# Optimization experiments

Hardware: AMD Instinct MI355X
Metric: run time of the kernel (lower is better)

The kernel has to match this reference:

```python
import jax, jax.numpy as jnp
import numpy as np
import math

B, H, W, DM = 4, 64, 64, 96
DS, DCONV, EXPAND = 16, 3, 2
DI = EXPAND * DM
DTR = math.ceil(DM / 16)
K = 4
HID = 4 * DI


def layernorm(x, g, b, eps=1e-5):
    m = x.mean(-1, keepdims=True)
    v = ((x - m) ** 2).mean(-1, keepdims=True)
    return (x - m) / jnp.sqrt(v + eps) * g + b


def dwconv(x, w, b=None):
    # x: (B,C,H,W), w: (C,1,kh,kw) depthwise, odd kernel => SAME padding == k//2
    out = jax.lax.conv_general_dilated(x, w, (1, 1), 'SAME',
                                       feature_group_count=x.shape[1],
                                       dimension_numbers=('NCHW', 'OIHW', 'NCHW'))
    if b is not None:
        out = out + b[None, :, None, None]
    return out


def ss2d_core(xc, x_proj_w, dt_projs_w, dt_projs_b, A_logs, Ds):
    # xc: (b, d_inner, h, w) -> (b, d_inner, L) summed over 4 scan directions
    b, c, h, w = xc.shape
    L = h * w
    x_hw = xc.reshape(b, c, L)
    x_wh = xc.transpose(0, 1, 3, 2).reshape(b, c, L)
    xs = jnp.stack([x_hw, x_wh], axis=1)                 # (b,2,c,L)
    xs = jnp.concatenate([xs, jnp.flip(xs, -1)], axis=1)  # (b,4,c,L)
    x_dbl = jnp.einsum('bkdl,kcd->bkcl', xs, x_proj_w)
    dts, Bs, Cs = jnp.split(x_dbl, [DTR, DTR + DS], axis=2)
    dts = jnp.einsum('bkrl,kdr->bkdl', dts, dt_projs_w)
    delta = jax.nn.softplus(dts + dt_projs_b[None, :, :, None])  # (b,K,c,L)
    A = -jnp.exp(A_logs).reshape(K, c, DS)                       # (K,c,n)

    def step(hst, inp):
        x_t, d_t, B_t, C_t = inp  # (b,K,c),(b,K,c),(b,K,n),(b,K,n)
        dA = jnp.exp(d_t[..., None] * A)                       # (b,K,c,n)
        hst = hst * dA + (d_t * x_t)[..., None] * B_t[:, :, None, :]
        y = jnp.einsum('bkdn,bkn->bkd', hst, C_t)
        return hst, y

    seq = (jnp.moveaxis(xs, -1, 0), jnp.moveaxis(delta, -1, 0),
           jnp.moveaxis(Bs, -1, 0), jnp.moveaxis(Cs, -1, 0))
    h0 = jnp.zeros((b, K, c, DS), xc.dtype)
    _, ys = jax.lax.scan(step, h0, seq)          # (L,b,K,c)
    ys = jnp.moveaxis(ys, 0, -1)                 # (b,K,c,L)
    ys = ys + Ds.reshape(K, c)[None, :, :, None] * xs
    y1 = ys[:, 0]
    inv = jnp.flip(ys[:, 2:4], -1)
    y2 = inv[:, 0]
    wh = ys[:, 1].reshape(b, c, w, h).swapaxes(2, 3).reshape(b, c, L)
    invwh = inv[:, 1].reshape(b, c, w, h).swapaxes(2, 3).reshape(b, c, L)
    return y1 + y2 + wh + invwh


def msffn(y, in_w, in_b, dw1, dw3, dw5, ln_g, ln_b, out_w, out_b):
    hcl = jax.nn.silu(y @ in_w.T + in_b)          # (b,h,w,HID)
    hc = hcl.transpose(0, 3, 1, 2)
    hc = hc + dwconv(hc, dw1) + dwconv(hc, dw3) + dwconv(hc, dw5)
    hn = layernorm(hc.transpose(0, 2, 3, 1), ln_g, ln_b)
    return hn @ out_w.T + out_b


def setup_inputs() -> dict:
    key = jax.random.key(0)
    ks = jax.random.split(key, 16)
    dt_init_std = DTR ** -0.5
    dt = jnp.exp(jax.random.uniform(ks[0], (K, DI)) * (math.log(0.1) - math.log(0.001)) + math.log(0.001))
    dt = jnp.clip(dt, 1e-4, None)
    inv_dt = dt + jnp.log(-jnp.expm1(-dt))          # softplus-inverse init for dt bias
    A_logs = jnp.tile(jnp.log(jnp.arange(1, DS + 1, dtype=jnp.float32))[None, :], (K * DI, 1))
    r = lambda i, sh, s: jax.random.normal(ks[i], sh, jnp.float32) * s
    return {
        'x': r(1, (B, H, W, DM), 1.0),
        'in_proj_w': r(2, (2 * DI, DM), DM ** -0.5),
        'conv_w': r(3, (DI, 1, DCONV, DCONV), 0.2),
        'conv_b': jnp.zeros((DI,), jnp.float32),
        'x_proj_w': r(4, (K, DTR + 2 * DS, DI), DI ** -0.5),
        'dt_projs_w': jax.random.uniform(ks[5], (K, DI, DTR), minval=-dt_init_std, maxval=dt_init_std),
        'dt_projs_b': inv_dt,
        'A_logs': A_logs,
        'Ds': jnp.ones((K * DI,), jnp.float32),
        'out_norm_g': jnp.ones((DI,), jnp.float32),
        'out_norm_b': jnp.zeros((DI,), jnp.float32),
        'out_proj_w': r(6, (DM, DI), DI ** -0.5),
        'ffn_in_w': r(7, (HID, DI), DI ** -0.5),
        'ffn_in_b': jnp.zeros((HID,), jnp.float32),
        'ffn_dw1': r(8, (HID, 1, 1, 1), 0.3),
        'ffn_dw3': r(9, (HID, 1, 3, 3), 0.2),
        'ffn_dw5': r(10, (HID, 1, 5, 5), 0.1),
        'ffn_ln_g': jnp.ones((HID,), jnp.float32),
        'ffn_ln_b': jnp.zeros((HID,), jnp.float32),
        'ffn_out_w': r(11, (DM, HID), HID ** -0.5),
        'ffn_out_b': jnp.zeros((DM,), jnp.float32),
        'skip_scale': jnp.ones((1,), jnp.float32),
    }


def reference(x, in_proj_w, conv_w, conv_b, x_proj_w, dt_projs_w, dt_projs_b, A_logs, Ds,
              out_norm_g, out_norm_b, out_proj_w, ffn_in_w, ffn_in_b, ffn_dw1, ffn_dw3,
              ffn_dw5, ffn_ln_g, ffn_ln_b, ffn_out_w, ffn_out_b, skip_scale):
    b, h, w, _ = x.shape
    xz = x @ in_proj_w.T                          # (b,h,w,2*DI)
    xi, z = jnp.split(xz, 2, axis=-1)
    xc = jax.nn.silu(dwconv(xi.transpose(0, 3, 1, 2), conv_w, conv_b))  # (b,DI,h,w)
    y = ss2d_core(xc, x_proj_w, dt_projs_w, dt_projs_b, A_logs, Ds)     # (b,DI,L)
    y = y.swapaxes(1, 2).reshape(b, h, w, DI)
    y = layernorm(y, out_norm_g, out_norm_b)
    y = y * jax.nn.silu(z)
    out = y @ out_proj_w.T
    ffn = msffn(y, ffn_in_w, ffn_in_b, ffn_dw1, ffn_dw3, ffn_dw5,
                ffn_ln_g, ffn_ln_b, ffn_out_w, ffn_out_b)
    return out + skip_scale * ffn
```

## Files before the change

kernel.cpp:

```cpp
#include <hip/hip_runtime.h>
#include <hip/hip_bf16.h>

constexpr int BB = 4, HH = 64, WW = 64, DMv = 96;
constexpr int DSn = 16, DIv = 192, DTRv = 6, KKv = 4, HIDv = 768;
constexpr int LL = 4096;
constexpr int NC = 32, CHK = LL / NC;
constexpr int NR = BB * LL;
constexpr int XDS = 40;

constexpr size_t S_xi   = (size_t)BB * LL * DIv;
constexpr size_t S_xdbl = (size_t)BB * KKv * LL * XDS;
constexpr size_t S_big  = (size_t)BB * KKv * LL * DIv;
constexpr size_t S_sp   = (size_t)BB * KKv * NC * DIv * DSn;

typedef __attribute__((ext_vector_type(8))) short short8;
typedef __attribute__((ext_vector_type(4))) float floatx4;

__device__ __forceinline__ float sigf(float x) { return 1.f / (1.f + __expf(-x)); }
__device__ __forceinline__ float softp(float x) {
  return (x > 20.f) ? x : __logf(1.f + __expf(x));
}
__device__ __forceinline__ short bfbits(float v) {
  __hip_bfloat16 h = __float2bfloat16(v);
  return *(short*)&h;
}

__device__ __forceinline__ int lmap(int k, int l) {
  int lr = (k & 2) ? (LL - 1 - l) : l;
  return (k & 1) ? (((lr & 63) << 6) | (lr >> 6)) : lr;
}

__global__ void k_wprep(const float* __restrict__ fiw, const float* __restrict__ opw,
                        const float* __restrict__ fow, const float* __restrict__ in_w,
                        const float* __restrict__ xpw, const float* __restrict__ x,
                        float* __restrict__ fiwT, float* __restrict__ opwT,
                        float* __restrict__ fowT, float* __restrict__ wt,
                        float* __restrict__ wcatT, float* __restrict__ xt,
                        short* __restrict__ fiwP) {
  int bx = blockIdx.x, t = threadIdx.x;
  __shared__ float smbuf[32 * 65];
  if (bx >= 1152) {
    int f = (bx - 1152) * 4 + (t >> 6);
    int lane = t & 63, ln16 = lane & 15, qd = lane >> 4;
    int kt = f / 48, ntg = f % 48;
    int n = ntg * 16 + ln16;
#pragma unroll
    for (int j = 0; j < 8; ++j) {
      int k = kt * 32 + qd * 8 + j;
      fiwP[(size_t)f * 512 + lane * 8 + j] = bfbits(fiw[(size_t)n * DIv + k]);
    }
    return;
  }
  if (bx >= 384) {
    int i4 = bx - 384;
    int r0 = (i4 / 3) * 64, k0 = (i4 % 3) * 32;
    float (*tile)[65] = (float(*)[65])smbuf;
#pragma unroll
    for (int ii = 0; ii < 8; ++ii) {
      int i = (t >> 5) + ii * 8, j = t & 31;
      tile[j][i] = x[(size_t)(r0 + i) * 96 + k0 + j];
    }
    __syncthreads();
#pragma unroll
    for (int jj = 0; jj < 8; ++jj) {
      int j = (t >> 6) + jj * 4, i = t & 63;
      xt[(size_t)(k0 + j) * NR + r0 + i] = tile[j][i];
    }
    return;
  }
  if (bx >= 270) {
    int idx = (bx - 270) * 256 + t;
    if (idx < 2 * 192 * 76) {
      int p = idx / (192 * 76);
      int rem = idx % (192 * 76);
      int d = rem / 76, j = rem % 76;
      int k = (j >= 38 ? 2 : 0) + p;
      int c = (j >= 38) ? j - 38 : j;
      wcatT[idx] = xpw[((size_t)(k * 38 + c)) * DIv + d];
    }
    return;
  }
  const float* src; float* dst; int R, C, r0, c0;
  if (bx < 144)      { src = fiw;  dst = fiwT; R = 768; C = 192; r0 = (bx / 6) * 32;         c0 = (bx % 6) * 32; }
  else if (bx < 162) { int i = bx - 144; src = opw; dst = opwT; R = 96;  C = 192; r0 = (i / 6) * 32;  c0 = (i % 6) * 32; }
  else if (bx < 234) { int i = bx - 162; src = fow; dst = fowT; R = 96;  C = 768; r0 = (i / 24) * 32; c0 = (i % 24) * 32; }
  else               { int i = bx - 234; src = in_w; dst = wt;  R = 384; C = 96;  r0 = (i / 3) * 32;  c0 = (i % 3) * 32; }
  float (*tile)[33] = (float(*)[33])smbuf;
  int tc = t & 31, tr = t >> 5;
#pragma unroll
  for (int i = 0; i < 4; ++i) {
    int r = r0 + tr + i * 8;
    if (r < R && c0 + tc < C) tile[tr + i * 8][tc] = src[(size_t)r * C + c0 + tc];
  }
  __syncthreads();
#pragma unroll
  for (int i = 0; i < 4; ++i) {
    int c = c0 + tr + i * 8;
    int r = r0 + tc;
    if (c < C && r < R) dst[(size_t)c * R + r] = tile[tc][tr + i * 8];
  }
}

__global__ void k_inproj(const float* __restrict__ xt, const float* __restrict__ wt,
                         float* __restrict__ xi, float* __restrict__ z) {
  int t = threadIdx.x;
  int wv = t >> 6, lane = t & 63;
  int rq = blockIdx.x * 256 + wv * 64 + lane;
  int c0 = blockIdx.y * 8;
  const float4* xt4 = (const float4*)xt;
  float4 acc[8];
#pragma unroll
  for (int c = 0; c < 8; ++c) acc[c] = make_float4(0.f, 0.f, 0.f, 0.f);
  for (int k = 0; k < 96; ++k) {
    float4 xv = xt4[(size_t)k * (NR / 4) + rq];
    const float* wr = wt + k * 384 + c0;
#pragma unroll
    for (int c = 0; c < 8; ++c) {
      float w = wr[c];
      acc[c].x += w * xv.x; acc[c].y += w * xv.y;
      acc[c].z += w * xv.z; acc[c].w += w * xv.w;
    }
  }
  float* dst; int cc;
  if (c0 < DIv) { dst = xi; cc = c0; } else { dst = z; cc = c0 - DIv; }
#pragma unroll
  for (int li = 0; li < 4; ++li) {
    size_t row = (size_t)rq * 4 + li;
    float4 v0, v1;
    v0.x = (&acc[0].x)[li]; v0.y = (&acc[1].x)[li];
    v0.z = (&acc[2].x)[li]; v0.w = (&acc[3].x)[li];
    v1.x = (&acc[4].x)[li]; v1.y = (&acc[5].x)[li];
    v1.z = (&acc[6].x)[li]; v1.w = (&acc[7].x)[li];
    float4* o4 = (float4*)(dst + row * DIv + cc);
    o4[0] = v0; o4[1] = v1;
  }
}

constexpr int TW2 = 18;
__global__ void k_dwconv3(const float* __restrict__ xi, const float* __restrict__ cw,
                          const float* __restrict__ cb, float* __restrict__ xc,
                          float* __restrict__ xcT, float* __restrict__ xcTs) {
  int tile = blockIdx.x;
  int cg = blockIdx.y, b = blockIdx.z;
  int t = threadIdx.x;
  int ti0 = (tile >> 2) * 16, tj0 = (tile & 3) * 16;
  __shared__ float sm[TW2 * TW2 * 32];

  for (int e = t; e < TW2 * TW2 * 32; e += 256) {
    int ec = e & 31;
    int sp = e >> 5;
    int hi = sp / TW2, hj = sp % TW2;
    int gi = ti0 + hi - 1, gj = tj0 + hj - 1;
    float v = 0.f;
    if ((unsigned)gi < (unsigned)HH && (unsigned)gj < (unsigned)WW)
      v = xi[((size_t)b * LL + gi * WW + gj) * DIv + cg * 32 + ec];
    sm[e] = v;
  }

  int c = t & 31, s0 = t >> 5;
  int cglob = cg * 32 + c;
  float wc[9];
#pragma unroll
  for (int j = 0; j < 9; ++j) wc[j] = cw[cglob * 9 + j];
  float bv = cb[cglob];
  __syncthreads();

  float res[32];
  for (int i = 0; i < 32; ++i) {
    int p = s0 + (i << 3);
    int r = p >> 4, q = p & 15;
    float s = bv;
#pragma unroll
    for (int di = 0; di < 3; ++di)
#pragma unroll
      for (int dj = 0; dj < 3; ++dj)
        s += sm[((r + di) * TW2 + (q + dj)) * 32 + c] * wc[di * 3 + dj];
    res[i] = s * sigf(s);
  }
  __syncthreads();
  for (int i = 0; i < 32; ++i) {
    int p = s0 + (i << 3);
    sm[p * 35 + c] = res[i];
  }
  __syncthreads();
  for (int it = 0; it < 32; ++it) {
    int e = it * 256 + t;
    int p = e >> 5, ec = e & 31;
    int l = (ti0 + (p >> 4)) * WW + tj0 + (p & 15);
    xc[((size_t)b * LL + l) * DIv + cg * 32 + ec] = sm[p * 35 + ec];
  }
  for (int d2 = 0; d2 < 32; ++d2) {
    int l = (ti0 + (t >> 4)) * WW + tj0 + (t & 15);
    xcT[(size_t)(cg * 32 + d2) * NR + b * LL + l] = sm[t * 35 + d2];
  }
  for (int d2 = 0; d2 < 32; ++d2) {
    int gjo = t >> 4, gio = t & 15;
    int lt2 = (tj0 + gjo) * WW + ti0 + gio;
    int p = gio * 16 + gjo;
    xcTs[(size_t)(cg * 32 + d2) * NR + b * LL + lt2] = sm[p * 35 + d2];
  }
}

__global__ void k_xdbl2(const float* __restrict__ xcT, const float* __restrict__ xcTs,
                        const float* __restrict__ wcatT, float* __restrict__ xdbl) {
  int t = threadIdx.x;
  int rq = blockIdx.x * 256 + t;
  int jg = blockIdx.y;
  int pb = blockIdx.z;
  int p = pb >> 2, b = pb & 3;
  const float4* A = (const float4*)(p ? xcTs : xcT);
  const float* wbase = wcatT + (size_t)p * 192 * 76 + jg * 4;
  float4 acc[4];
#pragma unroll
  for (int j = 0; j < 4; ++j) acc[j] = make_float4(0.f, 0.f, 0.f, 0.f);
  for (int d = 0; d < 192; ++d) {
    float4 xv = A[(size_t)d * (NR / 4) + b * 1024 + rq];
    const float* wr = wbase + d * 76;
#pragma unroll
    for (int j = 0; j < 4; ++j) {
      float w = wr[j];
      acc[j].x += w * xv.x; acc[j].y += w * xv.y;
      acc[j].z += w * xv.z; acc[j].w += w * xv.w;
    }
  }
#pragma unroll
  for (int li = 0; li < 4; ++li) {
    int r = rq * 4 + li;
#pragma unroll
    for (int j = 0; j < 4; ++j) {
      int col = jg * 4 + j;
      int kk = (col >= 38) ? (2 + p) : p;
      int c = (col >= 38) ? col - 38 : col;
      int l = (col >= 38) ? (LL - 1 - r) : r;
      int phys = c + (c >= 6 ? 2 : 0);
      size_t ro = (((size_t)(b * KKv + kk)) * LL + l) * XDS;
      xdbl[ro + phys] = (&acc[j].x)[li];
      if (col == 5) { xdbl[ro + 6] = 0.f; xdbl[ro + 7] = 0.f; }
    }
  }
}

__global__ void k_scan1(const float* __restrict__ xdbl, const float* __restrict__ xc,
                        const float* __restrict__ alogs, const float* __restrict__ dtw,
                        const float* __restrict__ dtb,
                        float* __restrict__ S, float* __restrict__ P) {
  int bx = blockIdx.x;
  int c = bx / 3, dblk = bx % 3;
  int k = blockIdx.y, b = blockIdx.z;
  int t = threadIdx.x, dl = t >> 2, nq = t & 3;
  int d = dblk * 64 + dl;
  __shared__ float de_s[16][64], xv_s[16][64], bc_s[16][32], dt_s[16][8];
  float A[4];
#pragma unroll
  for (int j = 0; j < 4; ++j)
    A[j] = -__expf(alogs[(size_t)(k * DIv + d) * DSn + nq * 4 + j]);
  int derow = t >> 4, dec0 = (t & 15) * 4;
  float DTW[4][6], DTB[4];
#pragma unroll
  for (int jj = 0; jj < 4; ++jj) {
    int dd = k * DIv + dblk * 64 + dec0 + jj;
    DTB[jj] = dtb[dd];
#pragma unroll
    for (int r2 = 0; r2 < 6; ++r2) DTW[jj][r2] = dtw[(size_t)dd * 6 + r2];
  }
  size_t bkL = (size_t)(b * KKv + k) * LL;
  const float* xq = xdbl + bkL * XDS;
  const float* xcb = xc + (size_t)b * LL * DIv;
  float h[4] = {0.f, 0.f, 0.f, 0.f}, sA[4] = {0.f, 0.f, 0.f, 0.f};
  int l0 = c * CHK;
  for (int tile = 0; tile < CHK / 16; ++tile) {
    int lt = l0 + tile * 16;
    __syncthreads();
    {
      int r = t >> 4, q = t & 15;
      int lc = lmap(k, lt + r);
      *(float4*)&xv_s[r][q * 4] = *(const float4*)(xcb + (size_t)lc * DIv + dblk * 64 + q * 4);
      if (t < 128) {
        int r2 = t >> 3, q2 = t & 7;
        *(float4*)&bc_s[r2][q2 * 4] = *(const float4*)(xq + (size_t)(lt + r2) * XDS + 8 + q2 * 4);
      } else if (t < 160) {
        int i3 = t - 128, r3 = i3 >> 1, half = i3 & 1;
        *(float4*)&dt_s[r3][half * 4] = *(const float4*)(xq + (size_t)(lt + r3) * XDS + half * 4);
      }
    }
    __syncthreads();
    {
#pragma unroll
      for (int jj = 0; jj < 4; ++jj) {
        float s = DTB[jj];
#pragma unroll
        for (int r2 = 0; r2 < 6; ++r2) s += dt_s[derow][r2] * DTW[jj][r2];
        de_s[derow][dec0 + jj] = softp(s);
      }
    }
    __syncthreads();
#pragma unroll
    for (int i2 = 0; i2 < 16; ++i2) {
      float de = de_s[i2][dl];
      float xv = xv_s[i2][dl];
      float4 Bv = *(float4*)&bc_s[i2][nq * 4];
      float db = de * xv;
#pragma unroll
      for (int j = 0; j < 4; ++j) {
        float u = de * A[j];
        sA[j] += u;
        h[j] = h[j] * __expf(u) + db * (&Bv.x)[j];
      }
    }
  }
  size_t o = ((((size_t)(b * KKv + k) * NC + c) * 3 + dblk) * 1024) + (size_t)t * 4;
  float4 hs, ps;
#pragma unroll
  for (int j = 0; j < 4; ++j) { (&hs.x)[j] = h[j]; (&ps.x)[j] = __expf(sA[j]); }
  *(float4*)(S + o) = hs;
  *(float4*)(P + o) = ps;
}

__global__ void k_scan2(float* __restrict__ S, const float* __restrict__ P) {
  int dblk = blockIdx.x, k = blockIdx.y, b = blockIdx.z;
  int t = threadIdx.x;
  size_t base = (((size_t)(b * KKv + k) * NC) * 3 + dblk) * 1024 + (size_t)t * 4;
  float4 h = make_float4(0.f, 0.f, 0.f, 0.f);
  for (int c = 0; c < NC; ++c) {
    size_t o = base + (size_t)c * 3 * 1024;
    float4 s = *(float4*)(S + o), p = *(float4*)(P + o);
    *(float4*)(S + o) = h;
    h.x = s.x + p.x * h.x; h.y = s.y + p.y * h.y;
    h.z = s.z + p.z * h.z; h.w = s.w + p.w * h.w;
  }
}

__global__ void k_scan3(const float* __restrict__ xdbl, const float* __restrict__ xc,
                        const float* __restrict__ alogs, const float* __restrict__ dtw,
                        const float* __restrict__ dtb,
                        const float* __restrict__ Hin, float* __restrict__ ys) {
  int bx = blockIdx.x;
  int c = bx / 3, dblk = bx % 3;
  int k = blockIdx.y, b = blockIdx.z;
  int t = threadIdx.x, dl = t >> 2, nq = t & 3;
  int d = dblk * 64 + dl;
  __shared__ float de_s[16][64], xv_s[16][64], bc_s[16][32], dt_s[16][8];
  float A[4];
#pragma unroll
  for (int j = 0; j < 4; ++j)
    A[j] = -__expf(alogs[(size_t)(k * DIv + d) * DSn + nq * 4 + j]);
  int derow = t >> 4, dec0 = (t & 15) * 4;
  float DTW[4][6], DTB[4];
#pragma unroll
  for (int jj = 0; jj < 4; ++jj) {
    int dd = k * DIv + dblk * 64 + dec0 + jj;
    DTB[jj] = dtb[dd];
#pragma unroll
    for (int r2 = 0; r2 < 6; ++r2) DTW[jj][r2] = dtw[(size_t)dd * 6 + r2];
  }
  size_t bkL = (size_t)(b * KKv + k) * LL;
  const float* xq = xdbl + bkL * XDS;
  const float* xcb = xc + (size_t)b * LL * DIv;
  float* yp = ys + bkL * DIv + d;
  size_t o = ((((size_t)(b * KKv + k) * NC + c) * 3 + dblk) * 1024) + (size_t)t * 4;
  float4 h4 = *(const float4*)(Hin + o);
  float h[4] = {h4.x, h4.y, h4.z, h4.w};
  int l0 = c * CHK;
  for (int tile = 0; tile < CHK / 16; ++tile) {
    int lt = l0 + tile * 16;
    __syncthreads();
    {
      int r = t >> 4, q = t & 15;
      int lc = lmap(k, lt + r);
      *(float4*)&xv_s[r][q * 4] = *(const float4*)(xcb + (size_t)lc * DIv + dblk * 64 + q * 4);
      if (t < 128) {
        int r2 = t >> 3, q2 = t & 7;
        *(float4*)&bc_s[r2][q2 * 4] = *(const float4*)(xq + (size_t)(lt + r2) * XDS + 8 + q2 * 4);
      } else if (t < 160) {
        int i3 = t - 128, r3 = i3 >> 1, half = i3 & 1;
        *(float4*)&dt_s[r3][half * 4] = *(const float4*)(xq + (size_t)(lt + r3) * XDS + half * 4);
      }
    }
    __syncthreads();
    {
#pragma unroll
      for (int jj = 0; jj < 4; ++jj) {
        float s = DTB[jj];
#pragma unroll
        for (int r2 = 0; r2 < 6; ++r2) s += dt_s[derow][r2] * DTW[jj][r2];
        de_s[derow][dec0 + jj] = softp(s);
      }
    }
    __syncthreads();
#pragma unroll
    for (int i2 = 0; i2 < 16; ++i2) {
      float de = de_s[i2][dl];
      float xv = xv_s[i2][dl];
      float4 Bv = *(float4*)&bc_s[i2][nq * 4];
      float4 Cv = *(float4*)&bc_s[i2][16 + nq * 4];
      float db = de * xv;
      float p = 0.f;
#pragma unroll
      for (int j = 0; j < 4; ++j) {
        h[j] = h[j] * __expf(de * A[j]) + db * (&Bv.x)[j];
        p += h[j] * (&Cv.x)[j];
      }
      p += __shfl_down(p, 2, 4);
      p += __shfl_down(p, 1, 4);
      if (nq == 0) yp[(size_t)(lt + i2) * DIv] = p;
    }
  }
}

__global__ void k_comlnt(const float* __restrict__ ys, const float* __restrict__ xc,
                         const float* __restrict__ Ds, const float* __restrict__ z,
                         const float* __restrict__ g, const float* __restrict__ be,
                         float* __restrict__ ygtT, __hip_bfloat16* __restrict__ ygtB) {
  int bl0 = blockIdx.x * 32;
  int b = bl0 >> 12, l0 = bl0 & 4095;
  int t = threadIdx.x;
  __shared__ float vbuf[32 * 193];
  __shared__ float m_[32], rs_[32];
  __shared__ float tile[32][33];
  {
    int grp = t >> 6, lane6 = t & 63;
    size_t base = (size_t)b * KKv * LL * DIv;
#pragma unroll
    for (int i8 = 0; i8 < 8; ++i8) {
      int li = grp + i8 * 4;
      int l = l0 + li;
      int lT = ((l & 63) << 6) | (l >> 6);
      const float* r0 = ys + base + (size_t)l * DIv;
      const float* r2 = ys + base + ((size_t)2 * LL + (LL - 1 - l)) * DIv;
      const float* r1 = ys + base + ((size_t)1 * LL + lT) * DIv;
      const float* r3 = ys + base + ((size_t)3 * LL + (LL - 1 - lT)) * DIv;
      const float* xr = xc + ((size_t)b * LL + l) * DIv;
#pragma unroll
      for (int cc = 0; cc < 3; ++cc) {
        int d = lane6 + cc * 64;
        float sd = Ds[d] + Ds[DIv + d] + Ds[2 * DIv + d] + Ds[3 * DIv + d];
        vbuf[li * 193 + d] = r0[d] + r2[d] + r1[d] + r3[d] + sd * xr[d];
      }
    }
  }
  __syncthreads();
  {
    int r = t >> 3, q = t & 7;
    float s = 0.f, qq = 0.f;
#pragma unroll
    for (int j = 0; j < 24; ++j) {
      float v = vbuf[r * 193 + q + j * 8];
      s += v; qq += v * v;
    }
    s += __shfl_down(s, 4, 8); qq += __shfl_down(qq, 4, 8);
    s += __shfl_down(s, 2, 8); qq += __shfl_down(qq, 2, 8);
    s += __shfl_down(s, 1, 8); qq += __shfl_down(qq, 1, 8);
    if (q == 0) {
      float m = s / DIv;
      m_[r] = m;
      rs_[r] = rsqrtf(qq / DIv - m * m + 1e-5f);
    }
  }
  __syncthreads();
  int tc = t & 31, tr = t >> 5;
  for (int ch = 0; ch < 6; ++ch) {
    int c0 = ch * 32;
    float gg = g[c0 + tc], bb = be[c0 + tc];
    if (ch) __syncthreads();
#pragma unroll
    for (int i = 0; i < 4; ++i) {
      int r = tr + i * 8;
      float v = vbuf[r * 193 + c0 + tc];
      float zz = z[(size_t)(bl0 + r) * DIv + c0 + tc];
      float val = (v - m_[r]) * rs_[r] * gg + bb;
      float gated = val * zz * sigf(zz);
      tile[tc][r] = gated;
      ygtB[(size_t)(bl0 + r) * DIv + c0 + tc] = __float2bfloat16(gated);
    }
    __syncthreads();
#pragma unroll
    for (int i = 0; i < 4; ++i) {
      int cr = tr + i * 8;
      ygtT[(size_t)(c0 + cr) * NR + bl0 + tc] = tile[cr][tc];
    }
  }
}

__global__ void k_outp(const float* __restrict__ ygtT, const float* __restrict__ opwT,
                       float* __restrict__ out0) {
  int t = threadIdx.x;
  int r2 = blockIdx.x * 256 + t;
  int c0 = blockIdx.y * 4;
  const float2* x2 = (const float2*)ygtT;
  float2 acc[4];
#pragma unroll
  for (int c = 0; c < 4; ++c) acc[c] = make_float2(0.f, 0.f);
#pragma unroll 4
  for (int k = 0; k < DIv; ++k) {
    float2 xv = x2[(size_t)k * (NR / 2) + r2];
    const float* wr = opwT + k * DMv + c0;
#pragma unroll
    for (int c = 0; c < 4; ++c) {
      float w = wr[c];
      acc[c].x += w * xv.x; acc[c].y += w * xv.y;
    }
  }
#pragma unroll
  for (int li = 0; li < 2; ++li) {
    float4 v;
    v.x = (&acc[0].x)[li]; v.y = (&acc[1].x)[li];
    v.z = (&acc[2].x)[li]; v.w = (&acc[3].x)[li];
    *(float4*)(out0 + ((size_t)r2 * 2 + li) * DMv + c0) = v;
  }
}

__global__ void k_ffnmf(const __hip_bfloat16* __restrict__ ygtB,
                        const short* __restrict__ fiwP,
                        const float* __restrict__ bias, float* __restrict__ hcl) {
  int t = threadIdx.x;
  int wv = t >> 6, lane = t & 63;
  int ln16 = lane & 15, qd = lane >> 4;
  int m0 = blockIdx.x * 64 + wv * 16;
  int n0 = blockIdx.y * 64;
  int ntg0 = n0 >> 4;
  floatx4 acc[4];
  floatx4 zero4 = {0.f, 0.f, 0.f, 0.f};
#pragma unroll
  for (int nt = 0; nt < 4; ++nt) acc[nt] = zero4;
  const short* arow = (const short*)ygtB + (size_t)(m0 + ln16) * DIv + qd * 8;
#pragma unroll
  for (int kt = 0; kt < 6; ++kt) {
    short8 a = *(const short8*)(arow + kt * 32);
    const short* bb = fiwP + ((size_t)(kt * 48 + ntg0) * 64 + lane) * 8;
#pragma unroll
    for (int nt = 0; nt < 4; ++nt) {
      short8 bfr = *(const short8*)(bb + (size_t)nt * 512);
      acc[nt] = __builtin_amdgcn_mfma_f32_16x16x32_bf16(a, bfr, acc[nt], 0, 0, 0);
    }
  }
#pragma unroll
  for (int nt = 0; nt < 4; ++nt) {
    int col = n0 + nt * 16 + ln16;
    float bv = bias[col];
#pragma unroll
    for (int r = 0; r < 4; ++r) {
      int row = m0 + qd * 4 + r;
      float s = acc[nt][r] + bv;
      hcl[(size_t)row * HIDv + col] = s * sigf(s);
    }
  }
}

constexpr int TS = 16, CG = 32, TW = TS + 4;
__global__ void k_ffnconv2(const float* __restrict__ hcl, const float* __restrict__ w1,
                           const float* __restrict__ w3, const float* __restrict__ w5,
                           float* __restrict__ hc2) {
  int tile = blockIdx.x;
  int cg = blockIdx.y, b = blockIdx.z;
  int t = threadIdx.x;
  int ti0 = (tile >> 2) * TS, tj0 = (tile & 3) * TS;
  __shared__ float sm[TW * TW * CG];

  for (int e = t; e < TW * TW * CG; e += 256) {
    int ec = e & 31;
    int sp = e >> 5;
    int hi = sp / TW, hj = sp % TW;
    int gi = ti0 + hi - 2, gj = tj0 + hj - 2;
    float v = 0.f;
    if ((unsigned)gi < (unsigned)HH && (unsigned)gj < (unsigned)WW)
      v = hcl[((size_t)b * LL + gi * WW + gj) * HIDv + cg * CG + ec];
    sm[e] = v;
  }

  int c = t & 31;
  int cglob = cg * CG + c;
  float wc[25];
#pragma unroll
  for (int di = 0; di < 5; ++di)
#pragma unroll
    for (int dj = 0; dj < 5; ++dj) {
      float w = w5[cglob * 25 + di * 5 + dj];
      if (di >= 1 && di <= 3 && dj >= 1 && dj <= 3)
        w += w3[cglob * 9 + (di - 1) * 3 + (dj - 1)];
      if (di == 2 && dj == 2) w += 1.f + w1[cglob];
      wc[di * 5 + dj] = w;
    }
  __syncthreads();

  int q2 = t >> 5;
#pragma unroll
  for (int half = 0; half < 2; ++half) {
    int q = q2 + half * 8;
    float win[5][5];
#pragma unroll
    for (int di = 0; di < 4; ++di)
#pragma unroll
      for (int dj = 0; dj < 5; ++dj)
        win[di][dj] = sm[(di * TW + (q + dj)) * CG + c];
#pragma unroll
    for (int r = 0; r < 16; ++r) {
      int slot = (r + 4) % 5;
#pragma unroll
      for (int dj = 0; dj < 5; ++dj)
        win[slot][dj] = sm[(((r + 4) * TW) + (q + dj)) * CG + c];
      float s = 0.f;
#pragma unroll
      for (int di = 0; di < 5; ++di) {
        int wsl = (r + di) % 5;
#pragma unroll
        for (int dj = 0; dj < 5; ++dj)
          s += win[wsl][dj] * wc[di * 5 + dj];
      }
      hc2[((size_t)b * LL + (ti0 + r) * WW + (tj0 + q)) * HIDv + cglob] = s;
    }
  }
}

__global__ void k_ln2t(const float* __restrict__ hc2, const float* __restrict__ g,
                       const float* __restrict__ be, float* __restrict__ hnT) {
  int r0 = blockIdx.x * 32;
  int t = threadIdx.x;
  __shared__ float m_[32], rs_[32];
  __shared__ float tile[32][33];
  {
    int r = t >> 3, q = t & 7;
    const float4* row4 = (const float4*)(hc2 + (size_t)(r0 + r) * HIDv);
    float s = 0.f, qq = 0.f;
#pragma unroll
    for (int j = 0; j < 24; ++j) {
      float4 v = row4[q + j * 8];
      s += v.x + v.y + v.z + v.w;
      qq += v.x * v.x + v.y * v.y + v.z * v.z + v.w * v.w;
    }
    s += __shfl_down(s, 4, 8); qq += __shfl_down(qq, 4, 8);
    s += __shfl_down(s, 2, 8); qq += __shfl_down(qq, 2, 8);
    s += __shfl_down(s, 1, 8); qq += __shfl_down(qq, 1, 8);
    if (q == 0) {
      float m = s / HIDv;
      m_[r] = m;
      rs_[r] = rsqrtf(qq / HIDv - m * m + 1e-5f);
    }
  }
  __syncthreads();
  int tc = t & 31, tr = t >> 5;
  for (int ch = 0; ch < 24; ++ch) {
    int c0 = ch * 32;
    float gg = g[c0 + tc], bb = be[c0 + tc];
    if (ch) __syncthreads();
#pragma unroll
    for (int i = 0; i < 4; ++i) {
      int r = tr + i * 8;
      float v = hc2[(size_t)(r0 + r) * HIDv + c0 + tc];
      tile[tc][r] = (v - m_[r]) * rs_[r] * gg + bb;
    }
    __syncthreads();
#pragma unroll
    for (int i = 0; i < 4; ++i) {
      int cr = tr + i * 8;
      hnT[(size_t)(c0 + cr) * NR + r0 + tc] = tile[cr][tc];
    }
  }
}

__global__ void k_final3(const float* __restrict__ hnT, const float* __restrict__ fowT,
                         float* __restrict__ part) {
  int t = threadIdx.x;
  int rq = blockIdx.x * 128 + t;
  int c0 = blockIdx.y * 8;
  int ks = blockIdx.z;
  const float4* x4 = (const float4*)hnT;
  float4 acc[8];
#pragma unroll
  for (int c = 0; c < 8; ++c) acc[c] = make_float4(0.f, 0.f, 0.f, 0.f);
  int k0 = ks * 192;
#pragma unroll 4
  for (int k = k0; k < k0 + 192; ++k) {
    float4 xv = x4[(size_t)k * (NR / 4) + rq];
    const float* wr = fowT + k * DMv + c0;
#pragma unroll
    for (int c = 0; c < 8; ++c) {
      float w = wr[c];
      acc[c].x += w * xv.x; acc[c].y += w * xv.y;
      acc[c].z += w * xv.z; acc[c].w += w * xv.w;
    }
  }
  float* pb = part + (size_t)ks * NR * DMv;
#pragma unroll
  for (int li = 0; li < 4; ++li) {
    size_t row = (size_t)rq * 4 + li;
#pragma unroll
    for (int cc = 0; cc < 2; ++cc) {
      float4 v;
#pragma unroll
      for (int j = 0; j < 4; ++j) (&v.x)[j] = (&acc[cc * 4 + j].x)[li];
      *(float4*)(pb + row * DMv + c0 + cc * 4) = v;
    }
  }
}

__global__ void k_finred(const float* __restrict__ part, const float* __restrict__ out0,
                         const float* __restrict__ bias, const float* __restrict__ skip,
                         float* __restrict__ dout) {
  size_t i = (size_t)blockIdx.x * 256 + threadIdx.x;
  int cq = (int)(i % (DMv / 4));
  const float4* p4 = (const float4*)part;
  size_t npart = (size_t)NR * DMv / 4;
  float4 a = p4[i], b2 = p4[i + npart], c2 = p4[i + 2 * npart], d2 = p4[i + 3 * npart];
  float4 o = ((const float4*)out0)[i];
  float4 bi = ((const float4*)bias)[cq];
  float sk = skip[0];
  float4 r;
  r.x = o.x + sk * (a.x + b2.x + c2.x + d2.x + bi.x);
  r.y = o.y + sk * (a.y + b2.y + c2.y + d2.y + bi.y);
  r.z = o.z + sk * (a.z + b2.z + c2.z + d2.z + bi.z);
  r.w = o.w + sk * (a.w + b2.w + c2.w + d2.w + bi.w);
  ((float4*)dout)[i] = r;
}

extern "C" void kernel_launch(void* const* d_in, const int* in_sizes, int n_in,
                              void* d_out, int out_size, void* d_ws, size_t ws_size,
                              hipStream_t stream) {
  const float* x        = (const float*)d_in[0];
  const float* in_w     = (const float*)d_in[1];
  const float* conv_w   = (const float*)d_in[2];
  const float* conv_b   = (const float*)d_in[3];
  const float* xpw      = (const float*)d_in[4];
  const float* dtw      = (const float*)d_in[5];
  const float* dtb      = (const float*)d_in[6];
  const float* alogs    = (const float*)d_in[7];
  const float* Ds       = (const float*)d_in[8];
  const float* ong      = (const float*)d_in[9];
  const float* onb      = (const float*)d_in[10];
  const float* opw      = (const float*)d_in[11];
  const float* fiw      = (const float*)d_in[12];
  const float* fib      = (const float*)d_in[13];
  const float* dw1      = (const float*)d_in[14];
  const float* dw3      = (const float*)d_in[15];
  const float* dw5      = (const float*)d_in[16];
  const float* flg      = (const float*)d_in[17];
  const float* flb      = (const float*)d_in[18];
  const float* fow      = (const float*)d_in[19];
  const float* fob      = (const float*)d_in[20];
  const float* skip     = (const float*)d_in[21];

  float* ws    = (float*)d_ws;
  float* xi    = ws;
  float* z     = xi + S_xi;
  float* xc    = z + S_xi;
  float* xdbl  = xc + S_xi;
  float* scr   = xdbl + S_xdbl;
  float* ys    = scr + S_big;
  float* wtiny = ys + S_big;
  float* fiwT  = wtiny;
  float* opwT  = fiwT + 147456;
  float* fowT  = opwT + 18432;
  float* wcatT = fowT + 73728;
  float* wt    = wcatT + 29184;
  __hip_bfloat16* ygtB = (__hip_bfloat16*)(wt + 36864);
  short* fiwP  = (short*)((float*)(wt + 36864) + 1572864);

  float* xt = scr;
  k_wprep<<<1224, 256, 0, stream>>>(fiw, opw, fow, in_w, xpw, x,
                                    fiwT, opwT, fowT, wt, wcatT, xt, fiwP);

  dim3 gip(NR / 1024, 48);
  k_inproj<<<gip, 256, 0, stream>>>(xt, wt, xi, z);

  float* xcT  = ys;
  float* xcTs = ys + S_xi;
  dim3 gdw(16, DIv / 32, BB);
  k_dwconv3<<<gdw, 256, 0, stream>>>(xi, conv_w, conv_b, xc, xcT, xcTs);

  dim3 gxd(4, 19, 8);
  k_xdbl2<<<gxd, 256, 0, stream>>>(xcT, xcTs, wcatT, xdbl);

  float* Sbuf = xi;
  float* Pbuf = xi + S_sp;
  dim3 gs13(NC * 3, KKv, BB);
  dim3 gs2(3, KKv, BB);
  k_scan1<<<gs13, 256, 0, stream>>>(xdbl, xc, alogs, dtw, dtb, Sbuf, Pbuf);
  k_scan2<<<gs2, 256, 0, stream>>>(Sbuf, Pbuf);
  k_scan3<<<gs13, 256, 0, stream>>>(xdbl, xc, alogs, dtw, dtb, Sbuf, ys);

  float* ygtT = xi;
  k_comlnt<<<NR / 32, 256, 0, stream>>>(ys, xc, Ds, z, ong, onb, ygtT, ygtB);

  float* out0 = xdbl;
  float* hcl = scr;
  dim3 gop(NR / 512, DMv / 4);
  k_outp<<<gop, 256, 0, stream>>>(ygtT, opwT, out0);
  dim3 gmf(NR / 64, HIDv / 64);
  k_ffnmf<<<gmf, 256, 0, stream>>>(ygtB, fiwP, fib, hcl);

  float* hc2 = ys;
  dim3 gc(16, HIDv / CG, BB);
  k_ffnconv2<<<gc, 256, 0, stream>>>(hcl, dw1, dw3, dw5, hc2);

  float* hnT = scr;
  k_ln2t<<<NR / 32, 256, 0, stream>>>(hc2, flg, flb, hnT);

  float* part = xi;
  dim3 gfn(NR / 512, DMv / 8, 4);
  k_final3<<<gfn, 128, 0, stream>>>(hnT, fowT, part);
  k_finred<<<(NR * DMv / 4) / 256, 256, 0, stream>>>(part, out0, fob, skip, (float*)d_out);
}
```

Baseline: 471.9 us.

## Fuse out-proj and FFN output GEMMs into one split-bf16 MFMA kernel

Replaces the scalar fp32 out-projection, the transposed LN2 output, the split-K final GEMM and the reduction kernel with one MFMA kernel. That kernel computes both GEMMs using bf16 hi/lo splitting (three MFMAs per tile) and writes the final output directly. LN2 and the gating kernel now write row-major bf16 hi/lo pairs instead of fp32 transposed buffers. Weight prep packs opw/fow into MFMA fragment layout and drops the unused transposes. The aim is to cut scalar FMA work, the partial-sum traffic and two launches, at the cost of slightly reduced precision from the bf16x3 emulation.

Result: faster. 430.9 us (-8.7%).

```diff
diff --git a/kernel.cpp b/kernel.cpp
--- a/kernel.cpp
+++ b/kernel.cpp
@@ -14,6 +14,7 @@
 constexpr size_t S_sp   = (size_t)BB * KKv * NC * DIv * DSn;
 
 typedef __attribute__((ext_vector_type(8))) short short8;
+typedef __attribute__((ext_vector_type(4))) short short4v;
 typedef __attribute__((ext_vector_type(4))) float floatx4;
 
 __device__ __forceinline__ float sigf(float x) { return 1.f / (1.f + __expf(-x)); }
@@ -33,43 +34,26 @@
 __global__ void k_wprep(const float* __restrict__ fiw, const float* __restrict__ opw,
                         const float* __restrict__ fow, const float* __restrict__ in_w,
                         const float* __restrict__ xpw, const float* __restrict__ x,
-                        float* __restrict__ fiwT, float* __restrict__ opwT,
-                        float* __restrict__ fowT, float* __restrict__ wt,
-                        float* __restrict__ wcatT, float* __restrict__ xt,
-                        short* __restrict__ fiwP) {
+                        float* __restrict__ wt, float* __restrict__ wcatT,
+                        float* __restrict__ xt, short* __restrict__ fiwP,
+                        short* __restrict__ opwP, short* __restrict__ fowP) {
   int bx = blockIdx.x, t = threadIdx.x;
   __shared__ float smbuf[32 * 65];
-  if (bx >= 1152) {
-    int f = (bx - 1152) * 4 + (t >> 6);
-    int lane = t & 63, ln16 = lane & 15, qd = lane >> 4;
-    int kt = f / 48, ntg = f % 48;
-    int n = ntg * 16 + ln16;
-#pragma unroll
-    for (int j = 0; j < 8; ++j) {
-      int k = kt * 32 + qd * 8 + j;
-      fiwP[(size_t)f * 512 + lane * 8 + j] = bfbits(fiw[(size_t)n * DIv + k]);
-    }
+  if (bx < 36) {
+    int r0 = (bx / 3) * 32, c0 = (bx % 3) * 32;
+    float (*tile)[33] = (float(*)[33])smbuf;
+    int tc = t & 31, tr = t >> 5;
+#pragma unroll
+    for (int i = 0; i < 4; ++i)
+      tile[tr + i * 8][tc] = in_w[(size_t)(r0 + tr + i * 8) * 96 + c0 + tc];
+    __syncthreads();
+#pragma unroll
+    for (int i = 0; i < 4; ++i)
+      wt[(size_t)(c0 + tr + i * 8) * 384 + r0 + tc] = tile[tc][tr + i * 8];
     return;
   }
-  if (bx >= 384) {
-    int i4 = bx - 384;
-    int r0 = (i4 / 3) * 64, k0 = (i4 % 3) * 32;
-    float (*tile)[65] = (float(*)[65])smbuf;
-#pragma unroll
-    for (int ii = 0; ii < 8; ++ii) {
-      int i = (t >> 5) + ii * 8, j = t & 31;
-      tile[j][i] = x[(size_t)(r0 + i) * 96 + k0 + j];
-    }
-    __syncthreads();
-#pragma unroll
-    for (int jj = 0; jj < 8; ++jj) {
-      int j = (t >> 6) + jj * 4, i = t & 63;
-      xt[(size_t)(k0 + j) * NR + r0 + i] = tile[j][i];
-    }
-    return;
-  }
-  if (bx >= 270) {
-    int idx = (bx - 270) * 256 + t;
+  if (bx < 150) {
+    int idx = (bx - 36) * 256 + t;
     if (idx < 2 * 192 * 76) {
       int p = idx / (192 * 76);
       int rem = idx % (192 * 76);
@@ -80,24 +64,63 @@
     }
     return;
   }
-  const float* src; float* dst; int R, C, r0, c0;
-  if (bx < 144)      { src = fiw;  dst = fiwT; R = 768; C = 192; r0 = (bx / 6) * 32;         c0 = (bx % 6) * 32; }
-  else if (bx < 162) { int i = bx - 144; src = opw; dst = opwT; R = 96;  C = 192; r0 = (i / 6) * 32;  c0 = (i % 6) * 32; }
-  else if (bx < 234) { int i = bx - 162; src = fow; dst = fowT; R = 96;  C = 768; r0 = (i / 24) * 32; c0 = (i % 24) * 32; }
-  else               { int i = bx - 234; src = in_w; dst = wt;  R = 384; C = 96;  r0 = (i / 3) * 32;  c0 = (i % 3) * 32; }
-  float (*tile)[33] = (float(*)[33])smbuf;
-  int tc = t & 31, tr = t >> 5;
-#pragma unroll
-  for (int i = 0; i < 4; ++i) {
-    int r = r0 + tr + i * 8;
-    if (r < R && c0 + tc < C) tile[tr + i * 8][tc] = src[(size_t)r * C + c0 + tc];
-  }
-  __syncthreads();
-#pragma unroll
-  for (int i = 0; i < 4; ++i) {
-    int c = c0 + tr + i * 8;
-    int r = r0 + tc;
-    if (c < C && r < R) dst[(size_t)c * R + r] = tile[tc][tr + i * 8];
+  if (bx < 918) {
+    int i4 = bx - 150;
+    int r0 = (i4 / 3) * 64, k0 = (i4 % 3) * 32;
+    float (*tile)[65] = (float(*)[65])smbuf;
+#pragma unroll
+    for (int ii = 0; ii < 8; ++ii) {
+      int i = (t >> 5) + ii * 8, j = t & 31;
+      tile[j][i] = x[(size_t)(r0 + i) * 96 + k0 + j];
+    }
+    __syncthreads();
+#pragma unroll
+    for (int jj = 0; jj < 8; ++jj) {
+      int j = (t >> 6) + jj * 4, i = t & 63;
+      xt[(size_t)(k0 + j) * NR + r0 + i] = tile[j][i];
+    }
+    return;
+  }
+  int lane = t & 63, ln16 = lane & 15, qd = lane >> 4;
+  if (bx < 990) {
+    int f = (bx - 918) * 4 + (t >> 6);
+    int kt = f / 48, ntg = f % 48;
+    int n = ntg * 16 + ln16;
+#pragma unroll
+    for (int j = 0; j < 8; ++j) {
+      int k = kt * 32 + qd * 8 + j;
+      fiwP[(size_t)f * 512 + lane * 8 + j] = bfbits(fiw[(size_t)n * DIv + k]);
+    }
+    return;
+  }
+  if (bx < 1008) {
+    int u = (bx - 990) * 4 + (t >> 6);
+    int f = u >> 1, part = u & 1;
+    int kt = f / 6, ntg = f % 6;
+    int n = ntg * 16 + ln16;
+#pragma unroll
+    for (int j = 0; j < 8; ++j) {
+      int k = kt * 32 + qd * 8 + j;
+      float w = opw[(size_t)n * DIv + k];
+      __hip_bfloat16 h = __float2bfloat16(w);
+      float v = part ? (w - (float)h) : w;
+      opwP[((size_t)(part * 36 + f)) * 512 + lane * 8 + j] = bfbits(v);
+    }
+    return;
+  }
+  {
+    int u = (bx - 1008) * 4 + (t >> 6);
+    int f = u >> 1, part = u & 1;
+    int kt = f / 6, ntg = f % 6;
+    int n = ntg * 16 + ln16;
+#pragma unroll
+    for (int j = 0; j < 8; ++j) {
+      int k = kt * 32 + qd * 8 + j;
+      float w = fow[(size_t)n * HIDv + k];
+      __hip_bfloat16 h = __float2bfloat16(w);
+      float v = part ? (w - (float)h) : w;
+      fowP[((size_t)(part * 144 + f)) * 512 + lane * 8 + j] = bfbits(v);
+    }
   }
 }
 
@@ -410,13 +433,13 @@
 __global__ void k_comlnt(const float* __restrict__ ys, const float* __restrict__ xc,
                          const float* __restrict__ Ds, const float* __restrict__ z,
                          const float* __restrict__ g, const float* __restrict__ be,
-                         float* __restrict__ ygtT, __hip_bfloat16* __restrict__ ygtB) {
+                         __hip_bfloat16* __restrict__ ygtB,
+                         __hip_bfloat16* __restrict__ ygtBl) {
   int bl0 = blockIdx.x * 32;
   int b = bl0 >> 12, l0 = bl0 & 4095;
   int t = threadIdx.x;
   __shared__ float vbuf[32 * 193];
   __shared__ float m_[32], rs_[32];
-  __shared__ float tile[32][33];
   {
     int grp = t >> 6, lane6 = t & 63;
     size_t base = (size_t)b * KKv * LL * DIv;
@@ -458,10 +481,10 @@
   }
   __syncthreads();
   int tc = t & 31, tr = t >> 5;
+#pragma unroll
   for (int ch = 0; ch < 6; ++ch) {
     int c0 = ch * 32;
     float gg = g[c0 + tc], bb = be[c0 + tc];
-    if (ch) __syncthreads();
 #pragma unroll
     for (int i = 0; i < 4; ++i) {
       int r = tr + i * 8;
@@ -469,43 +492,10 @@
       float zz = z[(size_t)(bl0 + r) * DIv + c0 + tc];
       float val = (v - m_[r]) * rs_[r] * gg + bb;
       float gated = val * zz * sigf(zz);
-      tile[tc][r] = gated;
-      ygtB[(size_t)(bl0 + r) * DIv + c0 + tc] = __float2bfloat16(gated);
-    }
-    __syncthreads();
-#pragma unroll
-    for (int i = 0; i < 4; ++i) {
-      int cr = tr + i * 8;
-      ygtT[(size_t)(c0 + cr) * NR + bl0 + tc] = tile[cr][tc];
-    }
-  }
-}
-
-__global__ void k_outp(const float* __restrict__ ygtT, const float* __restrict__ opwT,
-                       float* __restrict__ out0) {
-  int t = threadIdx.x;
-  int r2 = blockIdx.x * 256 + t;
-  int c0 = blockIdx.y * 4;
-  const float2* x2 = (const float2*)ygtT;
-  float2 acc[4];
-#pragma unroll
-  for (int c = 0; c < 4; ++c) acc[c] = make_float2(0.f, 0.f);
-#pragma unroll 4
-  for (int k = 0; k < DIv; ++k) {
-    float2 xv = x2[(size_t)k * (NR / 2) + r2];
-    const float* wr = opwT + k * DMv + c0;
-#pragma unroll
-    for (int c = 0; c < 4; ++c) {
-      float w = wr[c];
-      acc[c].x += w * xv.x; acc[c].y += w * xv.y;
-    }
-  }
-#pragma unroll
-  for (int li = 0; li < 2; ++li) {
-    float4 v;
-    v.x = (&acc[0].x)[li]; v.y = (&acc[1].x)[li];
-    v.z = (&acc[2].x)[li]; v.w = (&acc[3].x)[li];
-    *(float4*)(out0 + ((size_t)r2 * 2 + li) * DMv + c0) = v;
+      __hip_bfloat16 h = __float2bfloat16(gated);
+      ygtB[(size_t)(bl0 + r) * DIv + c0 + tc] = h;
+      ygtBl[(size_t)(bl0 + r) * DIv + c0 + tc] = __float2bfloat16(gated - (float)h);
+    }
   }
 }
 
@@ -611,25 +601,34 @@
   }
 }
 
-__global__ void k_ln2t(const float* __restrict__ hc2, const float* __restrict__ g,
-                       const float* __restrict__ be, float* __restrict__ hnT) {
-  int r0 = blockIdx.x * 32;
+constexpr int LNROWS = 16, LNPAD = 776;
+__global__ void k_ln2b(const float* __restrict__ hc2, const float* __restrict__ g,
+                       const float* __restrict__ be,
+                       short* __restrict__ hnBh, short* __restrict__ hnBl) {
+  int r0 = blockIdx.x * LNROWS;
   int t = threadIdx.x;
-  __shared__ float m_[32], rs_[32];
-  __shared__ float tile[32][33];
+  __shared__ float rows[LNROWS * LNPAD];
+  __shared__ float m_[LNROWS], rs_[LNROWS];
+#pragma unroll
+  for (int i = 0; i < 12; ++i) {
+    int idx4 = t + i * 256;
+    int row = idx4 / 192, c4 = idx4 % 192;
+    float4 v = *(const float4*)(hc2 + (size_t)(r0 + row) * HIDv + c4 * 4);
+    *(float4*)&rows[row * LNPAD + c4 * 4] = v;
+  }
+  __syncthreads();
   {
-    int r = t >> 3, q = t & 7;
-    const float4* row4 = (const float4*)(hc2 + (size_t)(r0 + r) * HIDv);
+    int r = t >> 4, q = t & 15;
     float s = 0.f, qq = 0.f;
 #pragma unroll
-    for (int j = 0; j < 24; ++j) {
-      float4 v = row4[q + j * 8];
-      s += v.x + v.y + v.z + v.w;
-      qq += v.x * v.x + v.y * v.y + v.z * v.z + v.w * v.w;
-    }
-    s += __shfl_down(s, 4, 8); qq += __shfl_down(qq, 4, 8);
-    s += __shfl_down(s, 2, 8); qq += __shfl_down(qq, 2, 8);
-    s += __shfl_down(s, 1, 8); qq += __shfl_down(qq, 1, 8);
+    for (int j = 0; j < 48; ++j) {
+      float v = rows[r * LNPAD + q + j * 16];
+      s += v; qq += v * v;
+    }
+    s += __shfl_down(s, 8, 16); qq += __shfl_down(qq, 8, 16);
+    s += __shfl_down(s, 4, 16); qq += __shfl_down(qq, 4, 16);
+    s += __shfl_down(s, 2, 16); qq += __shfl_down(qq, 2, 16);
+    s += __shfl_down(s, 1, 16); qq += __shfl_down(qq, 1, 16);
     if (q == 0) {
       float m = s / HIDv;
       m_[r] = m;
@@ -637,79 +636,88 @@
     }
   }
   __syncthreads();
-  int tc = t & 31, tr = t >> 5;
-  for (int ch = 0; ch < 24; ++ch) {
-    int c0 = ch * 32;
-    float gg = g[c0 + tc], bb = be[c0 + tc];
-    if (ch) __syncthreads();
-#pragma unroll
-    for (int i = 0; i < 4; ++i) {
-      int r = tr + i * 8;
-      float v = hc2[(size_t)(r0 + r) * HIDv + c0 + tc];
-      tile[tc][r] = (v - m_[r]) * rs_[r] * gg + bb;
-    }
-    __syncthreads();
-#pragma unroll
-    for (int i = 0; i < 4; ++i) {
-      int cr = tr + i * 8;
-      hnT[(size_t)(c0 + cr) * NR + r0 + tc] = tile[cr][tc];
-    }
-  }
-}
-
-__global__ void k_final3(const float* __restrict__ hnT, const float* __restrict__ fowT,
-                         float* __restrict__ part) {
+#pragma unroll
+  for (int i = 0; i < 12; ++i) {
+    int idx4 = t + i * 256;
+    int row = idx4 / 192, c4 = idx4 % 192;
+    float4 v = *(const float4*)&rows[row * LNPAD + c4 * 4];
+    float4 gv = *(const float4*)(g + c4 * 4);
+    float4 bv = *(const float4*)(be + c4 * 4);
+    float m = m_[row], rs = rs_[row];
+    short4v hh, ll;
+#pragma unroll
+    for (int j = 0; j < 4; ++j) {
+      float val = ((&v.x)[j] - m) * rs * (&gv.x)[j] + (&bv.x)[j];
+      __hip_bfloat16 h = __float2bfloat16(val);
+      hh[j] = *(short*)&h;
+      ll[j] = bfbits(val - (float)h);
+    }
+    size_t o = (size_t)(r0 + row) * HIDv + c4 * 4;
+    *(short4v*)(hnBh + o) = hh;
+    *(short4v*)(hnBl + o) = ll;
+  }
+}
+
+__global__ void k_finalmf(const short* __restrict__ hnBh, const short* __restrict__ hnBl,
+                          const short* __restrict__ fowP,
+                          const short* __restrict__ ygtBh, const short* __restrict__ ygtBl,
+                          const short* __restrict__ opwP,
+                          const float* __restrict__ fob, const float* __restrict__ skip,
+                          float* __restrict__ dout) {
   int t = threadIdx.x;
-  int rq = blockIdx.x * 128 + t;
-  int c0 = blockIdx.y * 8;
-  int ks = blockIdx.z;
-  const float4* x4 = (const float4*)hnT;
-  float4 acc[8];
-#pragma unroll
-  for (int c = 0; c < 8; ++c) acc[c] = make_float4(0.f, 0.f, 0.f, 0.f);
-  int k0 = ks * 192;
+  int wv = t >> 6, lane = t & 63;
+  int ln16 = lane & 15, qd = lane >> 4;
+  int m0 = blockIdx.x * 64 + wv * 16;
+  int ntg0 = blockIdx.y * 3;
+  floatx4 accF[3], accO[3];
+  floatx4 zero4 = {0.f, 0.f, 0.f, 0.f};
+#pragma unroll
+  for (int nt = 0; nt < 3; ++nt) { accF[nt] = zero4; accO[nt] = zero4; }
+  const short* arh = hnBh + (size_t)(m0 + ln16) * HIDv + qd * 8;
+  const short* arl = hnBl + (size_t)(m0 + ln16) * HIDv + qd * 8;
 #pragma unroll 4
-  for (int k = k0; k < k0 + 192; ++k) {
-    float4 xv = x4[(size_t)k * (NR / 4) + rq];
-    const float* wr = fowT + k * DMv + c0;
-#pragma unroll
-    for (int c = 0; c < 8; ++c) {
-      float w = wr[c];
-      acc[c].x += w * xv.x; acc[c].y += w * xv.y;
-      acc[c].z += w * xv.z; acc[c].w += w * xv.w;
-    }
-  }
-  float* pb = part + (size_t)ks * NR * DMv;
-#pragma unroll
-  for (int li = 0; li < 4; ++li) {
-    size_t row = (size_t)rq * 4 + li;
-#pragma unroll
-    for (int cc = 0; cc < 2; ++cc) {
-      float4 v;
-#pragma unroll
-      for (int j = 0; j < 4; ++j) (&v.x)[j] = (&acc[cc * 4 + j].x)[li];
-      *(float4*)(pb + row * DMv + c0 + cc * 4) = v;
-    }
-  }
-}
-
-__global__ void k_finred(const float* __restrict__ part, const float* __restrict__ out0,
-                         const float* __restrict__ bias, const float* __restrict__ skip,
-                         float* __restrict__ dout) {
-  size_t i = (size_t)blockIdx.x * 256 + threadIdx.x;
-  int cq = (int)(i % (DMv / 4));
-  const float4* p4 = (const float4*)part;
-  size_t npart = (size_t)NR * DMv / 4;
-  float4 a = p4[i], b2 = p4[i + npart], c2 = p4[i + 2 * npart], d2 = p4[i + 3 * npart];
-  float4 o = ((const float4*)out0)[i];
-  float4 bi = ((const float4*)bias)[cq];
+  for (int kt = 0; kt < 24; ++kt) {
+    short8 ah = *(const short8*)(arh + kt * 32);
+    short8 al = *(const short8*)(arl + kt * 32);
+    const short* bh = fowP + ((size_t)(kt * 6 + ntg0) * 64 + lane) * 8;
+    const short* bl = fowP + ((size_t)(144 + kt * 6 + ntg0) * 64 + lane) * 8;
+#pragma unroll
+    for (int nt = 0; nt < 3; ++nt) {
+      short8 bhv = *(const short8*)(bh + (size_t)nt * 512);
+      short8 blv = *(const short8*)(bl + (size_t)nt * 512);
+      accF[nt] = __builtin_amdgcn_mfma_f32_16x16x32_bf16(ah, bhv, accF[nt], 0, 0, 0);
+      accF[nt] = __builtin_amdgcn_mfma_f32_16x16x32_bf16(al, bhv, accF[nt], 0, 0, 0);
+      accF[nt] = __builtin_amdgcn_mfma_f32_16x16x32_bf16(ah, blv, accF[nt], 0, 0, 0);
+    }
+  }
+  const short* orh = ygtBh + (size_t)(m0 + ln16) * DIv + qd * 8;
+  const short* orl = ygtBl + (size_t)(m0 + ln16) * DIv + qd * 8;
+#pragma unroll
+  for (int kt = 0; kt < 6; ++kt) {
+    short8 ah = *(const short8*)(orh + kt * 32);
+    short8 al = *(const short8*)(orl + kt * 32);
+    const short* bh = opwP + ((size_t)(kt * 6 + ntg0) * 64 + lane) * 8;
+    const short* bl = opwP + ((size_t)(36 + kt * 6 + ntg0) * 64 + lane) * 8;
+#pragma unroll
+    for (int nt = 0; nt < 3; ++nt) {
+      short8 bhv = *(const short8*)(bh + (size_t)nt * 512);
+      short8 blv = *(const short8*)(bl + (size_t)nt * 512);
+      accO[nt] = __builtin_amdgcn_mfma_f32_16x16x32_bf16(ah, bhv, accO[nt], 0, 0, 0);
+      accO[nt] = __builtin_amdgcn_mfma_f32_16x16x32_bf16(al, bhv, accO[nt], 0, 0, 0);
+      accO[nt] = __builtin_amdgcn_mfma_f32_16x16x32_bf16(ah, blv, accO[nt], 0, 0, 0);
+    }
+  }
   float sk = skip[0];
-  float4 r;
-  r.x = o.x + sk * (a.x + b2.x + c2.x + d2.x + bi.x);
-  r.y = o.y + sk * (a.y + b2.y + c2.y + d2.y + bi.y);
-  r.z = o.z + sk * (a.z + b2.z + c2.z + d2.z + bi.z);
-  r.w = o.w + sk * (a.w + b2.w + c2.w + d2.w + bi.w);
-  ((float4*)dout)[i] = r;
+#pragma unroll
+  for (int nt = 0; nt < 3; ++nt) {
+    int col = (ntg0 + nt) * 16 + ln16;
+    float bv = fob[col];
+#pragma unroll
+    for (int r = 0; r < 4; ++r) {
+      int row = m0 + qd * 4 + r;
+      dout[(size_t)row * DMv + col] = accO[nt][r] + sk * (accF[nt][r] + bv);
+    }
+  }
 }
 
 extern "C" void kernel_launch(void* const* d_in, const int* in_sizes, int n_in,
@@ -746,17 +754,16 @@
   float* scr   = xdbl + S_xdbl;
   float* ys    = scr + S_big;
   float* wtiny = ys + S_big;
-  float* fiwT  = wtiny;
-  float* opwT  = fiwT + 147456;
-  float* fowT  = opwT + 18432;
-  float* wcatT = fowT + 73728;
+  float* wcatT = wtiny;
   float* wt    = wcatT + 29184;
   __hip_bfloat16* ygtB = (__hip_bfloat16*)(wt + 36864);
-  short* fiwP  = (short*)((float*)(wt + 36864) + 1572864);
+  short* fiwP  = (short*)(wt + 36864) + (size_t)NR * DIv;
+  short* opwP  = fiwP + 288 * 512;
+  short* fowP  = opwP + 2 * 36 * 512;
 
   float* xt = scr;
-  k_wprep<<<1224, 256, 0, stream>>>(fiw, opw, fow, in_w, xpw, x,
-                                    fiwT, opwT, fowT, wt, wcatT, xt, fiwP);
+  k_wprep<<<1080, 256, 0, stream>>>(fiw, opw, fow, in_w, xpw, x,
+                                    wt, wcatT, xt, fiwP, opwP, fowP);
 
   dim3 gip(NR / 1024, 48);
   k_inproj<<<gip, 256, 0, stream>>>(xt, wt, xi, z);
@@ -777,13 +784,10 @@
   k_scan2<<<gs2, 256, 0, stream>>>(Sbuf, Pbuf);
   k_scan3<<<gs13, 256, 0, stream>>>(xdbl, xc, alogs, dtw, dtb, Sbuf, ys);
 
-  float* ygtT = xi;
-  k_comlnt<<<NR / 32, 256, 0, stream>>>(ys, xc, Ds, z, ong, onb, ygtT, ygtB);
-
-  float* out0 = xdbl;
+  __hip_bfloat16* ygtBl = (__hip_bfloat16*)xi;
+  k_comlnt<<<NR / 32, 256, 0, stream>>>(ys, xc, Ds, z, ong, onb, ygtB, ygtBl);
+
   float* hcl = scr;
-  dim3 gop(NR / 512, DMv / 4);
-  k_outp<<<gop, 256, 0, stream>>>(ygtT, opwT, out0);
   dim3 gmf(NR / 64, HIDv / 64);
   k_ffnmf<<<gmf, 256, 0, stream>>>(ygtB, fiwP, fib, hcl);
 
@@ -791,11 +795,12 @@
   dim3 gc(16, HIDv / CG, BB);
   k_ffnconv2<<<gc, 256, 0, stream>>>(hcl, dw1, dw3, dw5, hc2);
 
-  float* hnT = scr;
-  k_ln2t<<<NR / 32, 256, 0, stream>>>(hc2, flg, flb, hnT);
-
-  float* part = xi;
-  dim3 gfn(NR / 512, DMv / 8, 4);
-  k_final3<<<gfn, 128, 0, stream>>>(hnT, fowT, part);
-  k_finred<<<(NR * DMv / 4) / 256, 256, 0, stream>>>(part, out0, fob, skip, (float*)d_out);
-}
+  short* hnBh = (short*)scr;
+  short* hnBl = hnBh + (size_t)NR * HIDv;
+  k_ln2b<<<NR / LNROWS, 256, 0, stream>>>(hc2, flg, flb, hnBh, hnBl);
+
+  dim3 gfm(NR / 64, 2);
+  k_finalmf<<<gfm, 256, 0, stream>>>(hnBh, hnBl, fowP,
+                                     (const short*)ygtB, (const short*)ygtBl, opwP,
+                                     fob, skip, (float*)d_out);
+}
```
